# Performance work log

Hardware: AMD Instinct MI355X
Metric: run time of the kernel (lower is better)

Reference implementation:

```python
import jax, jax.numpy as jnp
import numpy as np

B, TQ, TV = 4, 256, 256
H, D, U = 512, 512, 256  # hidden_size, value_size, units


def setup_inputs() -> dict:
    key = jax.random.key(0)
    ks = jax.random.split(key, 8)
    s = 0.02
    return {
        "query": jax.random.normal(ks[0], (B, TQ, H), dtype=jnp.float32),
        "values": jax.random.normal(ks[1], (B, TV, D), dtype=jnp.float32),
        "W1": jax.random.normal(ks[2], (H, U), dtype=jnp.float32) * s,
        "b1": jnp.zeros((U,), dtype=jnp.float32),
        "W2": jax.random.normal(ks[3], (D, U), dtype=jnp.float32) * s,
        "b2": jnp.zeros((U,), dtype=jnp.float32),
        "V": jax.random.normal(ks[4], (U, 1), dtype=jnp.float32) * s,
        "bV": jnp.zeros((1,), dtype=jnp.float32),
    }


def reference(query, values, W1, b1, W2, b2, V, bV):
    # query: [B,Tq,H]  values: [B,Tv,D]
    q = jnp.einsum("bqh,hu->bqu", query, W1) + b1          # [B,Tq,U]
    v = jnp.einsum("bvd,du->bvu", values, W2) + b2          # [B,Tv,U]
    # tf.repeat over Tq is just a broadcast of v; same math without materializing repeats twice
    hidden = jnp.tanh(q[:, :, None, :] + v[:, None, :, :])  # [B,Tq,Tv,U]
    score = jnp.einsum("bqvu,u->bqv", hidden, V[:, 0]) + bV[0]  # [B,Tq,Tv]
    attn = jax.nn.softmax(score, axis=2)                    # softmax over Tv (axis=2 of score)
    context = jnp.einsum("bqv,bvd->bqd", attn, values)      # [B,Tq,D]
    return context, attn[..., None]                          # weights returned as [B,Tq,Tv,1] like TF
```

## Files before the change

kernel.cpp:

```cpp
#include <hip/hip_runtime.h>
#include <math.h>


typedef float f4 __attribute__((ext_vector_type(4)));
typedef float f2 __attribute__((ext_vector_type(2)));
typedef __attribute__((ext_vector_type(8))) short s8v;
typedef __attribute__((ext_vector_type(8))) unsigned short u8v;

#define B_    4
#define TQ_   256
#define TV_   256
#define D_    512
#define U_    256
#define KDIM  512
#define MROWS 1024

#define C2LOG2E 2.8853900817779268f

#define EVT_U16_OFF   524288
#define ATTN_U16_OFF  786432
#define VALT_U16_OFF 1048576

#if __has_builtin(__builtin_amdgcn_exp2f)
#define EXP2F(x) __builtin_amdgcn_exp2f(x)
#else
#define EXP2F(x) exp2f(x)
#endif
#if __has_builtin(__builtin_amdgcn_rcpf)
#define RCPF(x) __builtin_amdgcn_rcpf(x)
#else
#define RCPF(x) (1.0f / (x))
#endif

__device__ __forceinline__ unsigned short f2bf(float f) {
    union { float f; unsigned u; } v; v.f = f;
    return (unsigned short)((v.u + 0x7FFF + ((v.u >> 16) & 1)) >> 16);
}
__device__ __forceinline__ float bf2f(unsigned short h) {
    union { unsigned u; float f; } v; v.u = (unsigned)h << 16;
    return v.f;
}
__device__ __forceinline__ u8v pack8(const f4 a, const f4 b) {
    u8v o;
    o[0] = f2bf(a[0]); o[1] = f2bf(a[1]); o[2] = f2bf(a[2]); o[3] = f2bf(a[3]);
    o[4] = f2bf(b[0]); o[5] = f2bf(b[1]); o[6] = f2bf(b[2]); o[7] = f2bf(b[3]);
    return o;
}

__global__ __launch_bounds__(256) void proj_mfma(
    const float* __restrict__ query, const float* __restrict__ values,
    const float* __restrict__ W1, const float* __restrict__ b1,
    const float* __restrict__ W2, const float* __restrict__ b2,
    float* __restrict__ ws)
{
    const int tid = threadIdx.x;
    const int job = blockIdx.y;

    if (job == 2) {
        const int idx = blockIdx.x * 256 + tid;
        const int d   = idx & 511;
        const int vg  = (idx >> 9) & 31;
        const int b   = idx >> 14;
        const float* src = values + ((size_t)b * TV_ + vg * 8) * KDIM + d;
        unsigned short* valT = (unsigned short*)ws + VALT_U16_OFF;
        u8v o;
        #pragma unroll
        for (int j = 0; j < 8; ++j) o[j] = f2bf(src[(size_t)j * KDIM]);
        *(u8v*)(valT + ((size_t)b * D_ + d) * TV_ + vg * 8) = o;
        return;
    }

    __shared__ u8v Al[32][64];
    __shared__ u8v Bl[32][64];

    const int proj = job;
    const int x    = blockIdx.x;

    int m0, n0;
    if (proj == 0) { m0 = (x >> 3) * 32; n0 = (x & 7) * 32; }
    else           { m0 = (x & 7) * 32;  n0 = (x >> 3) * 32; }

    const int drow = tid >> 3;
    const int duc  = (tid & 7) * 8;
    const float* dsrc = (proj ? values + (size_t)(n0 + drow) * KDIM
                              : query  + (size_t)(m0 + drow) * KDIM) + duc * 8;

    const int gcol = tid & 31;
    const int gk0  = (tid >> 5) * 64;
    const float* gsrc = (proj ? W2 + (m0 + gcol) : W1 + (n0 + gcol))
                        + (size_t)gk0 * U_;

    u8v (*DIR)[64] = proj ? Bl : Al;
    u8v (*GAT)[64] = proj ? Al : Bl;

    f4 dv[16];
    #pragma unroll
    for (int j = 0; j < 16; ++j) dv[j] = *(const f4*)(dsrc + j * 4);
    float gv[64];
    #pragma unroll
    for (int j = 0; j < 64; ++j) gv[j] = gsrc[(size_t)j * U_];

    #pragma unroll
    for (int j = 0; j < 8; ++j)
        DIR[drow][(duc + j) ^ (drow & 7)] = pack8(dv[2 * j], dv[2 * j + 1]);
    #pragma unroll
    for (int g = 0; g < 8; ++g) {
        u8v o;
        #pragma unroll
        for (int j = 0; j < 8; ++j) o[j] = f2bf(gv[g * 8 + j]);
        GAT[gcol][((gk0 >> 3) + g) ^ (gcol & 7)] = o;
    }
    __syncthreads();

    f4 acc = {};
    const int w    = tid >> 6;
    const int l    = tid & 63;
    const int fr   = l & 15;
    const int fko  = l >> 4;
    const int band = (w & 1) * 16;
    const int colh = (w >> 1) * 16;
    const int ar   = band + fr;
    const int br   = colh + fr;

    #pragma unroll
    for (int s = 0; s < 16; ++s) {
        s8v af = *(const s8v*)&Al[ar][(fko + 4 * s) ^ (ar & 7)];
        s8v bf = *(const s8v*)&Bl[br][(fko + 4 * s) ^ (br & 7)];
        acc = __builtin_amdgcn_mfma_f32_16x16x32_bf16(af, bf, acc, 0, 0, 0);
    }

    const int orow = m0 + band + (l >> 4) * 4;
    const int ocol = n0 + colh + (l & 15);

    if (proj == 0) {
        float* E = ws;
        const float bias = b1[ocol];
        #pragma unroll
        for (int r = 0; r < 4; ++r)
            E[(size_t)(orow + r) * U_ + ocol] =
                EXP2F((acc[r] + bias) * C2LOG2E);
    } else {
        unsigned short* E = (unsigned short*)ws + EVT_U16_OFF;
        #pragma unroll
        for (int r = 0; r < 4; ++r)
            E[(size_t)(orow + r) * MROWS + ocol] =
                f2bf(EXP2F((acc[r] + b2[orow + r]) * C2LOG2E));
    }
}

__global__ __launch_bounds__(256) void score_softmax(
    const float* __restrict__ Vw, float* __restrict__ ws,
    float* __restrict__ out)
{
    __shared__ float redmin[4][2];
    __shared__ float redsum[4][2];

    const int tid = threadIdx.x;
    const int b  = blockIdx.y;
    const int q0 = blockIdx.x * 2;

    const float* eq0 = ws + (size_t)(b * TQ_ + q0) * U_;
    const float* eq1 = eq0 + U_;
    const unsigned short* evp =
        (const unsigned short*)ws + EVT_U16_OFF + (size_t)b * TV_ + tid;
    float* attn = out + (size_t)B_ * TQ_ * D_ + (size_t)(b * TQ_ + q0) * TV_;
    unsigned short* attnbf =
        (unsigned short*)ws + ATTN_U16_OFF + (size_t)(b * TQ_ + q0) * TV_;

    float evA[8], evB[8];
    #pragma unroll
    for (int i = 0; i < 8; ++i) evA[i] = bf2f(evp[(size_t)i * MROWS]);

    f2 p = {0.f, 0.f};
    const f2 one = {1.0f, 1.0f};

#define SGRP(BUF, G)                                                    \
    _Pragma("unroll")                                                   \
    for (int i = 0; i < 8; ++i) {                                       \
        const int u = (G) * 8 + i;                                      \
        f2 eq = {eq0[u], eq1[u]};                      \
        f2 ev2 = {BUF[i], BUF[i]};                                      \
        f2 den = eq * ev2 + one;                      \
        f2 r = {RCPF(den.x), RCPF(den.y)};                              \
        f2 wv = {Vw[u], Vw[u]};                             \
        p = wv * r + p;                               \
    }

    #pragma unroll
    for (int g = 0; g < 32; g += 2) {
        #pragma unroll
        for (int i = 0; i < 8; ++i)
            evB[i] = bf2f(evp[(size_t)((g + 1) * 8 + i) * MROWS]);
        SGRP(evA, g)
        if (g + 2 < 32) {
            #pragma unroll
            for (int i = 0; i < 8; ++i)
                evA[i] = bf2f(evp[(size_t)((g + 2) * 8 + i) * MROWS]);
        }
        SGRP(evB, g + 1)
    }
#undef SGRP

    const int w = tid >> 6, lane = tid & 63;
    float m0 = p.x, m1 = p.y;
    #pragma unroll
    for (int off = 32; off; off >>= 1) {
        m0 = fminf(m0, __shfl_xor(m0, off));
        m1 = fminf(m1, __shfl_xor(m1, off));
    }
    if (lane == 0) { redmin[w][0] = m0; redmin[w][1] = m1; }
    __syncthreads();
    m0 = fminf(fminf(redmin[0][0], redmin[1][0]),
               fminf(redmin[2][0], redmin[3][0]));
    m1 = fminf(fminf(redmin[0][1], redmin[1][1]),
               fminf(redmin[2][1], redmin[3][1]));

    float e0 = EXP2F((m0 - p.x) * C2LOG2E);
    float e1 = EXP2F((m1 - p.y) * C2LOG2E);

    float s0 = e0, s1 = e1;
    #pragma unroll
    for (int off = 32; off; off >>= 1) {
        s0 += __shfl_xor(s0, off);
        s1 += __shfl_xor(s1, off);
    }
    if (lane == 0) { redsum[w][0] = s0; redsum[w][1] = s1; }
    __syncthreads();
    s0 = redsum[0][0] + redsum[1][0] + redsum[2][0] + redsum[3][0];
    s1 = redsum[0][1] + redsum[1][1] + redsum[2][1] + redsum[3][1];

    const float a0 = e0 * (1.0f / s0);
    const float a1 = e1 * (1.0f / s1);
    attn[tid]        = a0;
    attn[TV_ + tid]  = a1;
    attnbf[tid]        = f2bf(a0);
    attnbf[TV_ + tid]  = f2bf(a1);
}

__global__ __launch_bounds__(256) void ctx_mfma(
    const float* __restrict__ ws_ro, float* __restrict__ out)
{
    __shared__ unsigned short Al[2][32][72];
    __shared__ unsigned short Bl[2][32][72];

    const int tid = threadIdx.x;
    const int b   = blockIdx.y;
    const int x   = blockIdx.x;
    const int m0  = (x >> 4) * 32;
    const int n0  = (x & 15) * 32;

    const int row  = tid >> 3;
    const int koff = (tid & 7) * 8;

    const unsigned short* attnbf =
        (const unsigned short*)ws_ro + ATTN_U16_OFF;
    const unsigned short* valT =
        (const unsigned short*)ws_ro + VALT_U16_OFF;

    const unsigned short* asrc =
        attnbf + ((size_t)(b * TQ_ + m0 + row)) * TV_ + koff;
    const unsigned short* bsrc =
        valT + ((size_t)(b * D_ + n0 + row)) * TV_ + koff;

    u8v a8, b8;

#define LOADC(S)                                                        \
    do {                                                                \
        a8 = *(const u8v*)(asrc + (S) * 64);                            \
        b8 = *(const u8v*)(bsrc + (S) * 64);                            \
    } while (0)

#define WRITEC(BUF)                                                     \
    do {                                                                \
        *(u8v*)&Al[BUF][row][koff] = a8;                                \
        *(u8v*)&Bl[BUF][row][koff] = b8;                                \
    } while (0)

    f4 acc = {};

    const int w    = tid >> 6;
    const int l    = tid & 63;
    const int fr   = l & 15;
    const int fk   = (l >> 4) * 8;
    const int band = (w & 1) * 16;
    const int colh = (w >> 1) * 16;

    LOADC(0);
    WRITEC(0);

    for (int s = 0; s < 4; ++s) {
        __syncthreads();
        if (s + 1 < 4) LOADC(s + 1);
        {
            const int bu = s & 1;
            s8v af0 = *(const s8v*)&Al[bu][band + fr][fk];
            s8v af1 = *(const s8v*)&Al[bu][band + fr][fk + 32];
            s8v bf0 = *(const s8v*)&Bl[bu][colh + fr][fk];
            s8v bf1 = *(const s8v*)&Bl[bu][colh + fr][fk + 32];
            acc = __builtin_amdgcn_mfma_f32_16x16x32_bf16(af0, bf0, acc, 0, 0, 0);
            acc = __builtin_amdgcn_mfma_f32_16x16x32_bf16(af1, bf1, acc, 0, 0, 0);
        }
        if (s + 1 < 4) WRITEC((s + 1) & 1);
    }
#undef LOADC
#undef WRITEC

    const int orow = m0 + band + (l >> 4) * 4;
    const int ocol = n0 + colh + (l & 15);
    float* C = out + (size_t)b * TQ_ * D_;

    #pragma unroll
    for (int r = 0; r < 4; ++r)
        C[(size_t)(orow + r) * D_ + ocol] = acc[r];
}

extern "C" void kernel_launch(void* const* d_in, const int* in_sizes, int n_in,
                              void* d_out, int out_size, void* d_ws, size_t ws_size,
                              hipStream_t stream) {
    const float* query  = (const float*)d_in[0];
    const float* values = (const float*)d_in[1];
    const float* W1     = (const float*)d_in[2];
    const float* b1     = (const float*)d_in[3];
    const float* W2     = (const float*)d_in[4];
    const float* b2     = (const float*)d_in[5];
    const float* Vw     = (const float*)d_in[6];
    float* out = (float*)d_out;
    float* ws  = (float*)d_ws;

    proj_mfma<<<dim3(256, 3), 256, 0, stream>>>(query, values, W1, b1, W2, b2, ws);
    score_softmax<<<dim3(TQ_ / 2, B_), 256, 0, stream>>>(Vw, ws, out);
    ctx_mfma<<<dim3(128, B_), 256, 0, stream>>>(ws, out);
}
```

Measured before the change: 36.72 us.

## Fuse bf16 conversion of attention and values into context MFMA kernel

After: 38.12 us. 3.8% more time.

```diff
diff --git a/kernel.cpp b/kernel.cpp
--- a/kernel.cpp
+++ b/kernel.cpp
@@ -18,8 +18,6 @@
 #define C2LOG2E 2.8853900817779268f
 
 #define EVT_U16_OFF   524288
-#define ATTN_U16_OFF  786432
-#define VALT_U16_OFF 1048576
 
 #if __has_builtin(__builtin_amdgcn_exp2f)
 #define EXP2F(x) __builtin_amdgcn_exp2f(x)
@@ -54,26 +52,11 @@
     float* __restrict__ ws)
 {
     const int tid = threadIdx.x;
-    const int job = blockIdx.y;
-
-    if (job == 2) {
-        const int idx = blockIdx.x * 256 + tid;
-        const int d   = idx & 511;
-        const int vg  = (idx >> 9) & 31;
-        const int b   = idx >> 14;
-        const float* src = values + ((size_t)b * TV_ + vg * 8) * KDIM + d;
-        unsigned short* valT = (unsigned short*)ws + VALT_U16_OFF;
-        u8v o;
-        #pragma unroll
-        for (int j = 0; j < 8; ++j) o[j] = f2bf(src[(size_t)j * KDIM]);
-        *(u8v*)(valT + ((size_t)b * D_ + d) * TV_ + vg * 8) = o;
-        return;
-    }
 
     __shared__ u8v Al[32][64];
     __shared__ u8v Bl[32][64];
 
-    const int proj = job;
+    const int proj = blockIdx.y;
     const int x    = blockIdx.x;
 
     int m0, n0;
@@ -164,8 +147,6 @@
     const unsigned short* evp =
         (const unsigned short*)ws + EVT_U16_OFF + (size_t)b * TV_ + tid;
     float* attn = out + (size_t)B_ * TQ_ * D_ + (size_t)(b * TQ_ + q0) * TV_;
-    unsigned short* attnbf =
-        (unsigned short*)ws + ATTN_U16_OFF + (size_t)(b * TQ_ + q0) * TV_;
 
     float evA[8], evB[8];
     #pragma unroll
@@ -229,19 +210,15 @@
     s0 = redsum[0][0] + redsum[1][0] + redsum[2][0] + redsum[3][0];
     s1 = redsum[0][1] + redsum[1][1] + redsum[2][1] + redsum[3][1];
 
-    const float a0 = e0 * (1.0f / s0);
-    const float a1 = e1 * (1.0f / s1);
-    attn[tid]        = a0;
-    attn[TV_ + tid]  = a1;
-    attnbf[tid]        = f2bf(a0);
-    attnbf[TV_ + tid]  = f2bf(a1);
+    attn[tid]       = e0 * (1.0f / s0);
+    attn[TV_ + tid] = e1 * (1.0f / s1);
 }
 
 __global__ __launch_bounds__(256) void ctx_mfma(
-    const float* __restrict__ ws_ro, float* __restrict__ out)
+    const float* __restrict__ values, float* __restrict__ out)
 {
-    __shared__ unsigned short Al[2][32][72];
-    __shared__ unsigned short Bl[2][32][72];
+    __shared__ u8v Al[32][32];
+    __shared__ u8v Bl[32][32];
 
     const int tid = threadIdx.x;
     const int b   = blockIdx.y;
@@ -249,61 +226,52 @@
     const int m0  = (x >> 4) * 32;
     const int n0  = (x & 15) * 32;
 
-    const int row  = tid >> 3;
-    const int koff = (tid & 7) * 8;
-
-    const unsigned short* attnbf =
-        (const unsigned short*)ws_ro + ATTN_U16_OFF;
-    const unsigned short* valT =
-        (const unsigned short*)ws_ro + VALT_U16_OFF;
-
-    const unsigned short* asrc =
-        attnbf + ((size_t)(b * TQ_ + m0 + row)) * TV_ + koff;
-    const unsigned short* bsrc =
-        valT + ((size_t)(b * D_ + n0 + row)) * TV_ + koff;
-
-    u8v a8, b8;
-
-#define LOADC(S)                                                        \
-    do {                                                                \
-        a8 = *(const u8v*)(asrc + (S) * 64);                            \
-        b8 = *(const u8v*)(bsrc + (S) * 64);                            \
-    } while (0)
-
-#define WRITEC(BUF)                                                     \
-    do {                                                                \
-        *(u8v*)&Al[BUF][row][koff] = a8;                                \
-        *(u8v*)&Bl[BUF][row][koff] = b8;                                \
-    } while (0)
+    const float* attn = out + (size_t)B_ * TQ_ * D_ + (size_t)b * TQ_ * TV_;
+    const float* valb = values + (size_t)b * TV_ * D_;
+
+    const int drow = tid >> 3;
+    const int duc  = (tid & 7) * 4;
+    const float* asrc = attn + (size_t)(m0 + drow) * TV_ + duc * 8;
+
+    const int gcol = tid & 31;
+    const int gk0  = (tid >> 5) * 32;
+    const float* bsrc = valb + (size_t)gk0 * D_ + n0 + gcol;
+
+    f4 av[8];
+    #pragma unroll
+    for (int j = 0; j < 8; ++j) av[j] = *(const f4*)(asrc + j * 4);
+    float bv[32];
+    #pragma unroll
+    for (int j = 0; j < 32; ++j) bv[j] = bsrc[(size_t)j * D_];
+
+    #pragma unroll
+    for (int j = 0; j < 4; ++j)
+        Al[drow][(duc + j) ^ (drow & 7)] = pack8(av[2 * j], av[2 * j + 1]);
+    #pragma unroll
+    for (int g = 0; g < 4; ++g) {
+        u8v o;
+        #pragma unroll
+        for (int j = 0; j < 8; ++j) o[j] = f2bf(bv[g * 8 + j]);
+        Bl[gcol][((gk0 >> 3) + g) ^ (gcol & 7)] = o;
+    }
+    __syncthreads();
 
     f4 acc = {};
-
     const int w    = tid >> 6;
     const int l    = tid & 63;
     const int fr   = l & 15;
-    const int fk   = (l >> 4) * 8;
+    const int fko  = l >> 4;
     const int band = (w & 1) * 16;
     const int colh = (w >> 1) * 16;
-
-    LOADC(0);
-    WRITEC(0);
-
-    for (int s = 0; s < 4; ++s) {
-        __syncthreads();
-        if (s + 1 < 4) LOADC(s + 1);
-        {
-            const int bu = s & 1;
-            s8v af0 = *(const s8v*)&Al[bu][band + fr][fk];
-            s8v af1 = *(const s8v*)&Al[bu][band + fr][fk + 32];
-            s8v bf0 = *(const s8v*)&Bl[bu][colh + fr][fk];
-            s8v bf1 = *(const s8v*)&Bl[bu][colh + fr][fk + 32];
-            acc = __builtin_amdgcn_mfma_f32_16x16x32_bf16(af0, bf0, acc, 0, 0, 0);
-            acc = __builtin_amdgcn_mfma_f32_16x16x32_bf16(af1, bf1, acc, 0, 0, 0);
-        }
-        if (s + 1 < 4) WRITEC((s + 1) & 1);
-    }
-#undef LOADC
-#undef WRITEC
+    const int ar   = band + fr;
+    const int br   = colh + fr;
+
+    #pragma unroll
+    for (int s = 0; s < 8; ++s) {
+        s8v af = *(const s8v*)&Al[ar][(fko + 4 * s) ^ (ar & 7)];
+        s8v bf = *(const s8v*)&Bl[br][(fko + 4 * s) ^ (br & 7)];
+        acc = __builtin_amdgcn_mfma_f32_16x16x32_bf16(af, bf, acc, 0, 0, 0);
+    }
 
     const int orow = m0 + band + (l >> 4) * 4;
     const int ocol = n0 + colh + (l & 15);
@@ -327,7 +295,7 @@
     float* out = (float*)d_out;
     float* ws  = (float*)d_ws;
 
-    proj_mfma<<<dim3(256, 3), 256, 0, stream>>>(query, values, W1, b1, W2, b2, ws);
+    proj_mfma<<<dim3(256, 2), 256, 0, stream>>>(query, values, W1, b1, W2, b2, ws);
     score_softmax<<<dim3(TQ_ / 2, B_), 256, 0, stream>>>(Vw, ws, out);
-    ctx_mfma<<<dim3(128, B_), 256, 0, stream>>>(ws, out);
-}
+    ctx_mfma<<<dim3(128, B_), 256, 0, stream>>>(values, out);
+}
```

## Load full K tile into swizzled LDS once instead of double-buffered k-loop

Applied to the files above, without the earlier changes.

Result: faster. 35.87 us, median of 2 (-2.3%).

```diff
diff --git a/kernel.cpp b/kernel.cpp
--- a/kernel.cpp
+++ b/kernel.cpp
@@ -231,17 +231,17 @@
 
     const float a0 = e0 * (1.0f / s0);
     const float a1 = e1 * (1.0f / s1);
-    attn[tid]        = a0;
-    attn[TV_ + tid]  = a1;
-    attnbf[tid]        = f2bf(a0);
-    attnbf[TV_ + tid]  = f2bf(a1);
+    attn[tid]         = a0;
+    attn[TV_ + tid]   = a1;
+    attnbf[tid]       = f2bf(a0);
+    attnbf[TV_ + tid] = f2bf(a1);
 }
 
 __global__ __launch_bounds__(256) void ctx_mfma(
     const float* __restrict__ ws_ro, float* __restrict__ out)
 {
-    __shared__ unsigned short Al[2][32][72];
-    __shared__ unsigned short Bl[2][32][72];
+    __shared__ u8v Al[32][32];
+    __shared__ u8v Bl[32][32];
 
     const int tid = threadIdx.x;
     const int b   = blockIdx.y;
@@ -249,61 +249,55 @@
     const int m0  = (x >> 4) * 32;
     const int n0  = (x & 15) * 32;
 
-    const int row  = tid >> 3;
-    const int koff = (tid & 7) * 8;
-
     const unsigned short* attnbf =
         (const unsigned short*)ws_ro + ATTN_U16_OFF;
     const unsigned short* valT =
         (const unsigned short*)ws_ro + VALT_U16_OFF;
 
+    const int row = tid >> 3;
+    const int uc0 = (tid & 7) * 4;
+
     const unsigned short* asrc =
-        attnbf + ((size_t)(b * TQ_ + m0 + row)) * TV_ + koff;
+        attnbf + ((size_t)(b * TQ_ + m0 + row)) * TV_ + uc0 * 8;
     const unsigned short* bsrc =
-        valT + ((size_t)(b * D_ + n0 + row)) * TV_ + koff;
-
-    u8v a8, b8;
-
-#define LOADC(S)                                                        \
-    do {                                                                \
-        a8 = *(const u8v*)(asrc + (S) * 64);                            \
-        b8 = *(const u8v*)(bsrc + (S) * 64);                            \
-    } while (0)
-
-#define WRITEC(BUF)                                                     \
-    do {                                                                \
-        *(u8v*)&Al[BUF][row][koff] = a8;                                \
-        *(u8v*)&Bl[BUF][row][koff] = b8;                                \
-    } while (0)
+        valT + ((size_t)(b * D_ + n0 + row)) * TV_ + uc0 * 8;
+
+    u8v a0 = *(const u8v*)(asrc);
+    u8v a1 = *(const u8v*)(asrc + 8);
+    u8v a2 = *(const u8v*)(asrc + 16);
+    u8v a3 = *(const u8v*)(asrc + 24);
+    u8v v0 = *(const u8v*)(bsrc);
+    u8v v1 = *(const u8v*)(bsrc + 8);
+    u8v v2 = *(const u8v*)(bsrc + 16);
+    u8v v3 = *(const u8v*)(bsrc + 24);
+
+    const int sw = row & 7;
+    Al[row][(uc0 + 0) ^ sw] = a0;
+    Al[row][(uc0 + 1) ^ sw] = a1;
+    Al[row][(uc0 + 2) ^ sw] = a2;
+    Al[row][(uc0 + 3) ^ sw] = a3;
+    Bl[row][(uc0 + 0) ^ sw] = v0;
+    Bl[row][(uc0 + 1) ^ sw] = v1;
+    Bl[row][(uc0 + 2) ^ sw] = v2;
+    Bl[row][(uc0 + 3) ^ sw] = v3;
+    __syncthreads();
 
     f4 acc = {};
-
     const int w    = tid >> 6;
     const int l    = tid & 63;
     const int fr   = l & 15;
-    const int fk   = (l >> 4) * 8;
+    const int fko  = l >> 4;
     const int band = (w & 1) * 16;
     const int colh = (w >> 1) * 16;
-
-    LOADC(0);
-    WRITEC(0);
-
-    for (int s = 0; s < 4; ++s) {
-        __syncthreads();
-        if (s + 1 < 4) LOADC(s + 1);
-        {
-            const int bu = s & 1;
-            s8v af0 = *(const s8v*)&Al[bu][band + fr][fk];
-            s8v af1 = *(const s8v*)&Al[bu][band + fr][fk + 32];
-            s8v bf0 = *(const s8v*)&Bl[bu][colh + fr][fk];
-            s8v bf1 = *(const s8v*)&Bl[bu][colh + fr][fk + 32];
-            acc = __builtin_amdgcn_mfma_f32_16x16x32_bf16(af0, bf0, acc, 0, 0, 0);
-            acc = __builtin_amdgcn_mfma_f32_16x16x32_bf16(af1, bf1, acc, 0, 0, 0);
-        }
-        if (s + 1 < 4) WRITEC((s + 1) & 1);
-    }
-#undef LOADC
-#undef WRITEC
+    const int ar   = band + fr;
+    const int br   = colh + fr;
+
+    #pragma unroll
+    for (int s = 0; s < 8; ++s) {
+        s8v af = *(const s8v*)&Al[ar][(fko + 4 * s) ^ (ar & 7)];
+        s8v bf = *(const s8v*)&Bl[br][(fko + 4 * s) ^ (br & 7)];
+        acc = __builtin_amdgcn_mfma_f32_16x16x32_bf16(af, bf, acc, 0, 0, 0);
+    }
 
     const int orow = m0 + band + (l >> 4) * 4;
     const int ocol = n0 + colh + (l & 15);
```
